# Kernel tuning notes

Measured on AMD Instinct MI355X. Metric: run time of the kernel, lower is better.

## Reference

```python
import jax, jax.numpy as jnp
import numpy as np

B, S, E = 4, 2048, 1024


def setup_inputs() -> dict:
    key = jax.random.key(0)
    ks = jax.random.split(key, 7)
    sc = 1.0 / np.sqrt(E)
    return {
        "embedded": jax.random.normal(ks[0], (B, S, E), dtype=jnp.float32),
        "Wk": jax.random.normal(ks[1], (E, E), dtype=jnp.float32) * sc,
        "bk": jax.random.normal(ks[2], (E,), dtype=jnp.float32) * 0.01,
        "Wq": jax.random.normal(ks[3], (E, E), dtype=jnp.float32) * sc,
        "bq": jax.random.normal(ks[4], (E,), dtype=jnp.float32) * 0.01,
        "Wv": jax.random.normal(ks[5], (E, E), dtype=jnp.float32) * sc,
        "bv": jax.random.normal(ks[6], (E,), dtype=jnp.float32) * 0.01,
    }


def reference(embedded, Wk, bk, Wq, bq, Wv, bv):
    # embedded: [B, S, E]
    K = embedded @ Wk.T + bk  # [B,S,E]
    Q = embedded @ Wq.T + bq
    V = embedded @ Wv.T + bv
    seq_len = K.shape[1]
    # score[b,i,j] = K_i . Q_j, scaled by 1/sqrt(seq_len) (as in original)
    scores = jnp.einsum('bie,bje->bij', K, Q) / jnp.sqrt(jnp.asarray(seq_len, K.dtype))
    # softmax over dim=-2 -> over the key index i
    W = jax.nn.softmax(scores, axis=-2)  # [B,S,S]
    # Y = (V^T @ W)^T -> Y[b,j,d] = sum_i V[b,i,d] * W[b,i,j]
    Y = jnp.einsum('bid,bij->bjd', V, W)  # [B,S,E]
    return Y
```

## Files before the change

### kernel.cpp

```cpp
#include <hip/hip_runtime.h>
#include <hip/hip_bf16.h>


typedef __bf16 bf16x8 __attribute__((ext_vector_type(8)));
typedef float  f32x4  __attribute__((ext_vector_type(4)));

__device__ __forceinline__ unsigned short f2bf(float f) {
    unsigned int u = __float_as_uint(f);
    u = (u + 0x7FFFu + ((u >> 16) & 1u)) >> 16;
    return (unsigned short)u;
}

__global__ __launch_bounds__(256)
void cvt_all(const float* __restrict__ X,  const float* __restrict__ Wq,
             const float* __restrict__ Wk, const float* __restrict__ Wv,
             unsigned short* __restrict__ Xb,  unsigned short* __restrict__ Wqb,
             unsigned short* __restrict__ Wkb, unsigned short* __restrict__ Wvb,
             float* __restrict__ l) {
    long i = (long)blockIdx.x * 256 + threadIdx.x;
    if (i < 8192) l[i] = 0.0f;
    const float* src; unsigned short* dst; long off;
    if (i < 2097152L) { src = X; dst = Xb; off = i; }
    else {
        long j = i - 2097152L;
        int w = (int)(j >> 18);
        off = j & 262143L;
        src = (w == 0) ? Wq : (w == 1) ? Wk : Wv;
        dst = (w == 0) ? Wqb : (w == 1) ? Wkb : Wvb;
    }
    float4 v = reinterpret_cast<const float4*>(src)[off];
    ushort4 o;
    o.x = f2bf(v.x); o.y = f2bf(v.y); o.z = f2bf(v.z); o.w = f2bf(v.w);
    reinterpret_cast<ushort4*>(dst)[off] = o;
}

#define GEMM_DECLS                                                      \
    const int t    = threadIdx.x;                                       \
    const int wave = t >> 6;                                            \
    const int lane = t & 63;                                            \
    const int quad = lane >> 4;                                         \
    const int lr   = lane & 15;                                         \
    const int wm   = (wave >> 1) * 64;                                  \
    const int wn   = (wave & 1) * 64;                                   \
    const int sx   = lr & 7;                                            \
    const int lrow = lane >> 3;                                         \
    const int gch  = ((lane & 7) ^ (lrow & 7)) * 8;

#define GEMM_KLOOP(Aptr, Bptr, LDA, LDB)                                \
    for (int k0 = 0; k0 < K; k0 += 64) {                                \
        _Pragma("unroll")                                               \
        for (int r = 0; r < 4; ++r) {                                   \
            const int rowb = wave * 8 + r * 32;                         \
            const int row  = rowb + lrow;                               \
            const long goffA = (long)(m0 + row) * (LDA) + k0 + gch;     \
            const long goffB = (long)(n0 + row) * (LDB) + k0 + gch;     \
            __builtin_amdgcn_global_load_lds(                           \
                (const __attribute__((address_space(1))) void*)((Aptr) + goffA), \
                (__attribute__((address_space(3))) void*)(&lsA[rowb * 64]), 16, 0, 0); \
            __builtin_amdgcn_global_load_lds(                           \
                (const __attribute__((address_space(1))) void*)((Bptr) + goffB), \
                (__attribute__((address_space(3))) void*)(&lsB[rowb * 64]), 16, 0, 0); \
        }                                                               \
        __syncthreads();                                                \
        _Pragma("unroll")                                               \
        for (int h = 0; h < 2; ++h) {                                   \
            const int cp = ((h * 4 + quad) ^ sx) * 8;                   \
            bf16x8 af[4], bfr[4];                                       \
            _Pragma("unroll")                                           \
            for (int i = 0; i < 4; ++i) {                               \
                af[i]  = __builtin_bit_cast(bf16x8,                     \
                          *reinterpret_cast<const uint4*>(&lsA[(wm + i * 16 + lr) * 64 + cp])); \
                bfr[i] = __builtin_bit_cast(bf16x8,                     \
                          *reinterpret_cast<const uint4*>(&lsB[(wn + i * 16 + lr) * 64 + cp])); \
            }                                                           \
            _Pragma("unroll")                                           \
            for (int i = 0; i < 4; ++i)                                 \
                _Pragma("unroll")                                       \
                for (int j = 0; j < 4; ++j)                             \
                    acc[i][j] = __builtin_amdgcn_mfma_f32_16x16x32_bf16(af[i], bfr[j], acc[i][j], 0, 0, 0); \
        }                                                               \
        __syncthreads();                                                \
    }

__global__ __launch_bounds__(256, 2)
void gemm_qkv(const unsigned short* __restrict__ Xb,
              const unsigned short* __restrict__ Wqb,
              const unsigned short* __restrict__ Wkb,
              const unsigned short* __restrict__ Wvb,
              const float* __restrict__ bq, const float* __restrict__ bk,
              const float* __restrict__ bv_,
              unsigned short* __restrict__ Qb, unsigned short* __restrict__ Kb,
              unsigned short* __restrict__ Vt)
{
    __shared__ unsigned short lsA[128 * 64];
    __shared__ unsigned short lsB[128 * 64];

    const int id  = blockIdx.x;
    const int g   = id & 7;
    const int jj  = id >> 3;
    const int xx  = jj & 7;
    const int yin = (jj >> 3) & 7;
    const int z   = jj >> 6;

    const unsigned short* A = Xb;
    const unsigned short* B = (z == 0) ? Wqb : (z == 1) ? Wkb : Wvb;
    const float* bias       = (z == 0) ? bq  : (z == 1) ? bk  : bv_;

    const int n0 = xx * 128;
    const int m0 = (g * 8 + yin) * 128;
    const int K = 1024;

    GEMM_DECLS
    f32x4 acc[4][4] = {};
    GEMM_KLOOP(A, B, 1024, 1024)

#pragma unroll
    for (int j = 0; j < 4; ++j) {
        const int n = n0 + wn + j * 16 + lr;
        const float bvv = bias[n];
#pragma unroll
        for (int i = 0; i < 4; ++i) {
            const int mbase = m0 + wm + i * 16 + quad * 4;
            if (z < 2) {
                unsigned short* C = (z == 0) ? Qb : Kb;
#pragma unroll
                for (int r = 0; r < 4; ++r)
                    C[(long)(mbase + r) * 1024 + n] = f2bf(acc[i][j][r] + bvv);
            } else {
                ushort4 o;
                o.x = f2bf(acc[i][j][0] + bvv);
                o.y = f2bf(acc[i][j][1] + bvv);
                o.z = f2bf(acc[i][j][2] + bvv);
                o.w = f2bf(acc[i][j][3] + bvv);
                long boff = (long)(mbase >> 11) * (1024L * 2048) + (long)n * 2048 + (mbase & 2047);
                *reinterpret_cast<ushort4*>(Vt + boff) = o;
            }
        }
    }
}

__global__ __launch_bounds__(256, 2)
void gemm_scores(const unsigned short* __restrict__ Q,
                 const unsigned short* __restrict__ Kp,
                 unsigned short* __restrict__ P, float* __restrict__ l,
                 float scale)
{
    __shared__ unsigned short lsA[128 * 64];
    __shared__ unsigned short lsB[128 * 64];

    const int id  = blockIdx.x;
    const int g   = id & 7;
    const int u   = id >> 3;
    const int bz  = g >> 1;
    const int mh  = g & 1;
    const int xx  = u & 15;
    const int yin = u >> 4;

    const unsigned short* A = Q  + (long)bz * 2048 * 1024;
    const unsigned short* B = Kp + (long)bz * 2048 * 1024;
    unsigned short* Pb = P + (long)bz * 2048 * 2048;
    float* lb = l + bz * 2048;

    const int n0 = xx * 128;
    const int m0 = (mh * 8 + yin) * 128;
    const int K = 1024;

    GEMM_DECLS
    f32x4 acc[4][4] = {};
    GEMM_KLOOP(A, B, 1024, 1024)

#pragma unroll
    for (int i = 0; i < 4; ++i) {
#pragma unroll
        for (int r = 0; r < 4; ++r) {
            const int m = m0 + wm + i * 16 + quad * 4 + r;
            float psum = 0.0f;
#pragma unroll
            for (int j = 0; j < 4; ++j) {
                const float p = __expf(acc[i][j][r] * scale);
                psum += p;
                const int n = n0 + wn + j * 16 + lr;
                Pb[(long)m * 2048 + n] = f2bf(p);
            }
#pragma unroll
            for (int o = 1; o < 16; o <<= 1) psum += __shfl_xor(psum, o, 64);
            if (lr == 0) atomicAdd(&lb[m], psum);
        }
    }
}

__global__ __launch_bounds__(256, 2)
void gemm_y(const unsigned short* __restrict__ P,
            const unsigned short* __restrict__ Vt,
            const float* __restrict__ l, float* __restrict__ out)
{
    __shared__ unsigned short lsA[128 * 64];
    __shared__ unsigned short lsB[128 * 64];

    const int id  = blockIdx.x;
    const int g   = id & 7;
    const int u   = id >> 3;
    const int bz  = g >> 1;
    const int mh  = g & 1;
    const int xx  = u & 7;
    const int yin = u >> 3;

    const unsigned short* A = P  + (long)bz * 2048 * 2048;
    const unsigned short* B = Vt + (long)bz * 1024 * 2048;
    const float* lb = l + bz * 2048;
    float* C = out + (long)bz * 2048 * 1024;

    const int n0 = xx * 128;
    const int m0 = (mh * 8 + yin) * 128;
    const int K = 2048;

    GEMM_DECLS
    f32x4 acc[4][4] = {};
    GEMM_KLOOP(A, B, 2048, 2048)

    float linv[4][4];
#pragma unroll
    for (int i = 0; i < 4; ++i)
#pragma unroll
        for (int r = 0; r < 4; ++r)
            linv[i][r] = 1.0f / lb[m0 + wm + i * 16 + quad * 4 + r];

#pragma unroll
    for (int j = 0; j < 4; ++j) {
        const int n = n0 + wn + j * 16 + lr;
#pragma unroll
        for (int i = 0; i < 4; ++i) {
            const int mbase = m0 + wm + i * 16 + quad * 4;
#pragma unroll
            for (int r = 0; r < 4; ++r)
                C[(long)(mbase + r) * 1024 + n] = acc[i][j][r] * linv[i][r];
        }
    }
}

extern "C" void kernel_launch(void* const* d_in, const int* in_sizes, int n_in,
                              void* d_out, int out_size, void* d_ws, size_t ws_size,
                              hipStream_t stream) {
    const float* X  = (const float*)d_in[0];
    const float* Wk = (const float*)d_in[1];
    const float* bk = (const float*)d_in[2];
    const float* Wq = (const float*)d_in[3];
    const float* bq = (const float*)d_in[4];
    const float* Wv = (const float*)d_in[5];
    const float* bv = (const float*)d_in[6];
    float* out = (float*)d_out;

    const size_t MB = 1024 * 1024;
    if (ws_size < 80 * MB) return;

    char* ws = (char*)d_ws;
    unsigned short* Vt  = (unsigned short*)(ws);
    unsigned short* P   = (unsigned short*)(ws + 16 * MB);
    unsigned short* Xbf = (unsigned short*)(ws + 16 * MB);
    float*          l   = (float*)(ws + 48 * MB);
    unsigned short* Wqb = (unsigned short*)(ws + 49 * MB);
    unsigned short* Wkb = (unsigned short*)(ws + 51 * MB);
    unsigned short* Wvb = (unsigned short*)(ws + 53 * MB);
    unsigned short* Qb = (unsigned short*)d_out;
    unsigned short* Kb = Qb + 8192L * 1024;

    dim3 blk(256);

    cvt_all<<<2883584 / 256, blk, 0, stream>>>(X, Wq, Wk, Wv, Xbf, Wqb, Wkb, Wvb, l);

    gemm_qkv<<<1536, blk, 0, stream>>>(Xbf, Wqb, Wkb, Wvb, bq, bk, bv, Qb, Kb, Vt);

    gemm_scores<<<1024, blk, 0, stream>>>(Qb, Kb, P, l, 0.022097086912079608f);

    gemm_y<<<512, blk, 0, stream>>>(P, Vt, l, out);
}
```

Before: 238.2 us.

## Rewrite GEMMs as 512-thread, 256-tile, double-buffered software-pipelined kernels

Replaces the simple load-sync-compute loop in all three GEMMs with a double-buffered, phase-interleaved pipeline. Each phase issues global-to-LDS loads for a later k-slice while MFMAs run, using explicit vmcnt waits, barriers and setprio. Tiles grow to 256x256 (256x128 for the output GEMM) with 8 waves per block, which raises data reuse and cuts the grid size. The cost is much larger LDS use (128 KB or 96 KB per block) and more accumulator registers, both of which may lower occupancy, plus fragile hand-written wait counts.

New measurement: 247.6 us. 1.04x slower.

```diff
diff --git a/kernel.cpp b/kernel.cpp
--- a/kernel.cpp
+++ b/kernel.cpp
@@ -34,55 +34,93 @@
     reinterpret_cast<ushort4*>(dst)[off] = o;
 }
 
-#define GEMM_DECLS                                                      \
-    const int t    = threadIdx.x;                                       \
-    const int wave = t >> 6;                                            \
-    const int lane = t & 63;                                            \
-    const int quad = lane >> 4;                                         \
-    const int lr   = lane & 15;                                         \
-    const int wm   = (wave >> 1) * 64;                                  \
-    const int wn   = (wave & 1) * 64;                                   \
-    const int sx   = lr & 7;                                            \
-    const int lrow = lane >> 3;                                         \
-    const int gch  = ((lane & 7) ^ (lrow & 7)) * 8;
-
-#define GEMM_KLOOP(Aptr, Bptr, LDA, LDB)                                \
-    for (int k0 = 0; k0 < K; k0 += 64) {                                \
-        _Pragma("unroll")                                               \
-        for (int r = 0; r < 4; ++r) {                                   \
-            const int rowb = wave * 8 + r * 32;                         \
-            const int row  = rowb + lrow;                               \
-            const long goffA = (long)(m0 + row) * (LDA) + k0 + gch;     \
-            const long goffB = (long)(n0 + row) * (LDB) + k0 + gch;     \
-            __builtin_amdgcn_global_load_lds(                           \
-                (const __attribute__((address_space(1))) void*)((Aptr) + goffA), \
-                (__attribute__((address_space(3))) void*)(&lsA[rowb * 64]), 16, 0, 0); \
-            __builtin_amdgcn_global_load_lds(                           \
-                (const __attribute__((address_space(1))) void*)((Bptr) + goffB), \
-                (__attribute__((address_space(3))) void*)(&lsB[rowb * 64]), 16, 0, 0); \
-        }                                                               \
-        __syncthreads();                                                \
-        _Pragma("unroll")                                               \
-        for (int h = 0; h < 2; ++h) {                                   \
-            const int cp = ((h * 4 + quad) ^ sx) * 8;                   \
-            bf16x8 af[4], bfr[4];                                       \
-            _Pragma("unroll")                                           \
-            for (int i = 0; i < 4; ++i) {                               \
-                af[i]  = __builtin_bit_cast(bf16x8,                     \
-                          *reinterpret_cast<const uint4*>(&lsA[(wm + i * 16 + lr) * 64 + cp])); \
-                bfr[i] = __builtin_bit_cast(bf16x8,                     \
-                          *reinterpret_cast<const uint4*>(&lsB[(wn + i * 16 + lr) * 64 + cp])); \
-            }                                                           \
-            _Pragma("unroll")                                           \
-            for (int i = 0; i < 4; ++i)                                 \
-                _Pragma("unroll")                                       \
-                for (int j = 0; j < 4; ++j)                             \
-                    acc[i][j] = __builtin_amdgcn_mfma_f32_16x16x32_bf16(af[i], bfr[j], acc[i][j], 0, 0, 0); \
-        }                                                               \
-        __syncthreads();                                                \
-    }
-
-__global__ __launch_bounds__(256, 2)
+
+#define VMW(N) asm volatile("s_waitcnt vmcnt(" #N ")" ::: "memory")
+
+#define PIPE_DECLS                                                          \
+    const int tid  = threadIdx.x;                                           \
+    const int wave = tid >> 6;                                              \
+    const int lane = tid & 63;                                              \
+    const int quad = lane >> 4;                                             \
+    const int lr   = lane & 15;                                             \
+    const int wvm  = wave >> 2;                           \
+    const int wvn  = wave & 3;                            \
+    const int rd_off = (lr >> 1) * 64 + (lr & 1) * 32                       \
+                     + ((quad ^ ((lr >> 1) & 3)) << 3);                     \
+    const int stg_rl = wave * 16 + ((lane >> 3) << 1) + ((lane >> 2) & 1);  \
+    const int stg_c  = (((lane & 3) ^ ((lane >> 3) & 3)) << 3);
+
+#define ST1(base, LD, kcol, dst, c)                                         \
+    __builtin_amdgcn_global_load_lds(                                       \
+        (const __attribute__((address_space(1))) void*)                     \
+            ((base) + (long)(c) * 128 * (LD) + (kcol)),                     \
+        (__attribute__((address_space(3))) void*)(&lds[(dst) + (c) * 4096 + wave * 512]), \
+        16, 0, 0)
+
+#define PHASE(bs, h, mh, IH_, STG, WAITS)                                   \
+    {                                                                       \
+        if ((mh) == 0) {                                                    \
+            _Pragma("unroll")                                               \
+            for (int j = 0; j < 4; ++j)                                     \
+                bfr[j] = __builtin_bit_cast(bf16x8,                         \
+                    *reinterpret_cast<const uint4*>(                        \
+                        &lds[BOFF(bs, h) + (wvn * 4 + j) * 512 + rd_off])); \
+        }                                                                   \
+        bf16x8 af[IH_];                                                     \
+        _Pragma("unroll")                                                   \
+        for (int i = 0; i < (IH_); ++i)                                     \
+            af[i] = __builtin_bit_cast(bf16x8,                              \
+                *reinterpret_cast<const uint4*>(                            \
+                    &lds[AOFF(bs, h) + (wvm * 2 * (IH_) + (mh) * (IH_) + i) * 512 + rd_off])); \
+        STG;                                                                \
+        WAITS;                                                              \
+        __builtin_amdgcn_s_barrier();                                       \
+        __builtin_amdgcn_s_setprio(1);                                      \
+        _Pragma("unroll")                                                   \
+        for (int i = 0; i < (IH_); ++i)                                     \
+            _Pragma("unroll")                                               \
+            for (int j = 0; j < 4; ++j)                                     \
+                acc[(mh) * (IH_) + i][j] = __builtin_amdgcn_mfma_f32_16x16x32_bf16( \
+                    af[i], bfr[j], acc[(mh) * (IH_) + i][j], 0, 0, 0);      \
+        __builtin_amdgcn_s_setprio(0);                                      \
+        __builtin_amdgcn_s_barrier();                                       \
+    }
+
+#define RUN_PIPELINE(IH_, NT_, WAITST)                                      \
+    f32x4 acc[2 * (IH_)][4] = {};                                           \
+    bf16x8 bfr[4];                                                          \
+    SA(0, 0, 0); SB(0, 0, 0); SA(0, 1, 0); SB(0, 1, 0); SA(1, 0, 1); SB(1, 0, 1); \
+    WAITST;                                                                 \
+    __builtin_amdgcn_s_barrier();                                           \
+    _Pragma("unroll 1")                                                     \
+    for (int it = 0; it < (NT_) / 2 - 1; ++it) {                            \
+        const int tb = 2 * it;                                              \
+        PHASE(0, 0, 0, IH_, SA(tb + 1, 1, 1), )                             \
+        PHASE(0, 0, 1, IH_, SB(tb + 1, 1, 1), )                             \
+        PHASE(0, 1, 0, IH_, SA(tb + 2, 0, 0), )                             \
+        PHASE(0, 1, 1, IH_, SB(tb + 2, 0, 0), WAITST)                       \
+        PHASE(1, 0, 0, IH_, SA(tb + 2, 1, 0), )                             \
+        PHASE(1, 0, 1, IH_, SB(tb + 2, 1, 0), )                             \
+        PHASE(1, 1, 0, IH_, SA(tb + 3, 0, 1), )                             \
+        PHASE(1, 1, 1, IH_, SB(tb + 3, 0, 1), WAITST)                       \
+    }                                                                       \
+    PHASE(0, 0, 0, IH_, SA((NT_) - 1, 1, 1), )                              \
+    PHASE(0, 0, 1, IH_, SB((NT_) - 1, 1, 1), )                              \
+    PHASE(0, 1, 0, IH_, , )                                                 \
+    PHASE(0, 1, 1, IH_, , WAITST)                                           \
+    PHASE(1, 0, 0, IH_, , )                                                 \
+    PHASE(1, 0, 1, IH_, , VMW(0))                                           \
+    PHASE(1, 1, 0, IH_, , )                                                 \
+    PHASE(1, 1, 1, IH_, , )
+
+#define AOFF(b, h) ((b) * 32768 + (h) * 8192)
+#define BOFF(b, h) ((b) * 32768 + 16384 + (h) * 8192)
+#define SA(tt, h, b) { ST1(aBase, 1024, (tt) * 64 + (h) * 32, AOFF(b, h), 0); \
+                       ST1(aBase, 1024, (tt) * 64 + (h) * 32, AOFF(b, h), 1); }
+#define SB(tt, h, b) { ST1(bBase, 1024, (tt) * 64 + (h) * 32, BOFF(b, h), 0); \
+                       ST1(bBase, 1024, (tt) * 64 + (h) * 32, BOFF(b, h), 1); }
+
+__global__ __launch_bounds__(512, 2)
 void gemm_qkv(const unsigned short* __restrict__ Xb,
               const unsigned short* __restrict__ Wqb,
               const unsigned short* __restrict__ Wkb,
@@ -92,35 +130,33 @@
               unsigned short* __restrict__ Qb, unsigned short* __restrict__ Kb,
               unsigned short* __restrict__ Vt)
 {
-    __shared__ unsigned short lsA[128 * 64];
-    __shared__ unsigned short lsB[128 * 64];
-
-    const int id  = blockIdx.x;
-    const int g   = id & 7;
-    const int jj  = id >> 3;
-    const int xx  = jj & 7;
-    const int yin = (jj >> 3) & 7;
-    const int z   = jj >> 6;
-
-    const unsigned short* A = Xb;
-    const unsigned short* B = (z == 0) ? Wqb : (z == 1) ? Wkb : Wvb;
-    const float* bias       = (z == 0) ? bq  : (z == 1) ? bk  : bv_;
-
-    const int n0 = xx * 128;
-    const int m0 = (g * 8 + yin) * 128;
-    const int K = 1024;
-
-    GEMM_DECLS
-    f32x4 acc[4][4] = {};
-    GEMM_KLOOP(A, B, 1024, 1024)
+    __shared__ __align__(16) unsigned short lds[65536];
+
+    const int id = blockIdx.x;
+    const int g  = id & 7;
+    const int u  = id >> 3;
+    const int z  = u >> 4;
+    const int w  = u & 15;
+    const int m0 = (g * 4 + (w >> 2)) * 256;
+    const int n0 = (w & 3) * 256;
+
+    const unsigned short* Aptr = Xb;
+    const unsigned short* Bptr = (z == 0) ? Wqb : (z == 1) ? Wkb : Wvb;
+    const float* bias          = (z == 0) ? bq  : (z == 1) ? bk  : bv_;
+
+    PIPE_DECLS
+    const unsigned short* aBase = Aptr + (long)(m0 + stg_rl) * 1024 + stg_c;
+    const unsigned short* bBase = Bptr + (long)(n0 + stg_rl) * 1024 + stg_c;
+
+    RUN_PIPELINE(4, 16, VMW(4))
 
 #pragma unroll
     for (int j = 0; j < 4; ++j) {
-        const int n = n0 + wn + j * 16 + lr;
+        const int n = n0 + wvn * 64 + j * 16 + lr;
         const float bvv = bias[n];
 #pragma unroll
-        for (int i = 0; i < 4; ++i) {
-            const int mbase = m0 + wm + i * 16 + quad * 4;
+        for (int i = 0; i < 8; ++i) {
+            const int mbase = m0 + wvm * 128 + i * 16 + quad * 4;
             if (z < 2) {
                 unsigned short* C = (z == 0) ? Qb : Kb;
 #pragma unroll
@@ -139,48 +175,43 @@
     }
 }
 
-__global__ __launch_bounds__(256, 2)
+__global__ __launch_bounds__(512, 2)
 void gemm_scores(const unsigned short* __restrict__ Q,
                  const unsigned short* __restrict__ Kp,
                  unsigned short* __restrict__ P, float* __restrict__ l,
                  float scale)
 {
-    __shared__ unsigned short lsA[128 * 64];
-    __shared__ unsigned short lsB[128 * 64];
-
-    const int id  = blockIdx.x;
-    const int g   = id & 7;
-    const int u   = id >> 3;
-    const int bz  = g >> 1;
-    const int mh  = g & 1;
-    const int xx  = u & 15;
-    const int yin = u >> 4;
-
-    const unsigned short* A = Q  + (long)bz * 2048 * 1024;
-    const unsigned short* B = Kp + (long)bz * 2048 * 1024;
+    __shared__ __align__(16) unsigned short lds[65536];
+
+    const int id = blockIdx.x;
+    const int g  = id & 7;
+    const int u  = id >> 3;
+    const int bz = g >> 1;
+    const int m0 = ((g & 1) * 4 + (u & 3)) * 256;
+    const int n0 = (u >> 2) * 256;
+
+    const unsigned short* Aptr = Q  + (long)bz * 2048 * 1024;
+    const unsigned short* Bptr = Kp + (long)bz * 2048 * 1024;
     unsigned short* Pb = P + (long)bz * 2048 * 2048;
     float* lb = l + bz * 2048;
 
-    const int n0 = xx * 128;
-    const int m0 = (mh * 8 + yin) * 128;
-    const int K = 1024;
-
-    GEMM_DECLS
-    f32x4 acc[4][4] = {};
-    GEMM_KLOOP(A, B, 1024, 1024)
-
-#pragma unroll
-    for (int i = 0; i < 4; ++i) {
+    PIPE_DECLS
+    const unsigned short* aBase = Aptr + (long)(m0 + stg_rl) * 1024 + stg_c;
+    const unsigned short* bBase = Bptr + (long)(n0 + stg_rl) * 1024 + stg_c;
+
+    RUN_PIPELINE(4, 16, VMW(4))
+
+#pragma unroll
+    for (int i = 0; i < 8; ++i) {
 #pragma unroll
         for (int r = 0; r < 4; ++r) {
-            const int m = m0 + wm + i * 16 + quad * 4 + r;
+            const int m = m0 + wvm * 128 + i * 16 + quad * 4 + r;
             float psum = 0.0f;
 #pragma unroll
             for (int j = 0; j < 4; ++j) {
                 const float p = __expf(acc[i][j][r] * scale);
                 psum += p;
-                const int n = n0 + wn + j * 16 + lr;
-                Pb[(long)m * 2048 + n] = f2bf(p);
+                Pb[(long)m * 2048 + (n0 + wvn * 64 + j * 16 + lr)] = f2bf(p);
             }
 #pragma unroll
             for (int o = 1; o < 16; o <<= 1) psum += __shfl_xor(psum, o, 64);
@@ -189,54 +220,66 @@
     }
 }
 
-__global__ __launch_bounds__(256, 2)
+#undef SA
+#undef SB
+#undef AOFF
+#undef BOFF
+
+#define AOFF(b, h) ((b) * 24576 + (h) * 4096)
+#define BOFF(b, h) ((b) * 24576 + 8192 + (h) * 8192)
+#define SA(tt, h, b) { ST1(aBase, 2048, (tt) * 64 + (h) * 32, AOFF(b, h), 0); }
+#define SB(tt, h, b) { ST1(bBase, 2048, (tt) * 64 + (h) * 32, BOFF(b, h), 0); \
+                       ST1(bBase, 2048, (tt) * 64 + (h) * 32, BOFF(b, h), 1); }
+
+__global__ __launch_bounds__(512, 2)
 void gemm_y(const unsigned short* __restrict__ P,
             const unsigned short* __restrict__ Vt,
             const float* __restrict__ l, float* __restrict__ out)
 {
-    __shared__ unsigned short lsA[128 * 64];
-    __shared__ unsigned short lsB[128 * 64];
-
-    const int id  = blockIdx.x;
-    const int g   = id & 7;
-    const int u   = id >> 3;
-    const int bz  = g >> 1;
-    const int mh  = g & 1;
-    const int xx  = u & 7;
-    const int yin = u >> 3;
-
-    const unsigned short* A = P  + (long)bz * 2048 * 2048;
-    const unsigned short* B = Vt + (long)bz * 1024 * 2048;
+    __shared__ __align__(16) unsigned short lds[49152];
+
+    const int id = blockIdx.x;
+    const int g  = id & 7;
+    const int u  = id >> 3;
+    const int bz = g >> 1;
+    const int m0 = ((g & 1) * 8 + (u & 7)) * 128;
+    const int n0 = (u >> 3) * 256;
+
+    const unsigned short* Aptr = P  + (long)bz * 2048 * 2048;
+    const unsigned short* Bptr = Vt + (long)bz * 1024 * 2048;
     const float* lb = l + bz * 2048;
     float* C = out + (long)bz * 2048 * 1024;
 
-    const int n0 = xx * 128;
-    const int m0 = (mh * 8 + yin) * 128;
-    const int K = 2048;
-
-    GEMM_DECLS
-    f32x4 acc[4][4] = {};
-    GEMM_KLOOP(A, B, 2048, 2048)
+    PIPE_DECLS
+    const unsigned short* aBase = Aptr + (long)(m0 + stg_rl) * 2048 + stg_c;
+    const unsigned short* bBase = Bptr + (long)(n0 + stg_rl) * 2048 + stg_c;
+
+    RUN_PIPELINE(2, 32, VMW(3))
 
     float linv[4][4];
 #pragma unroll
     for (int i = 0; i < 4; ++i)
 #pragma unroll
         for (int r = 0; r < 4; ++r)
-            linv[i][r] = 1.0f / lb[m0 + wm + i * 16 + quad * 4 + r];
+            linv[i][r] = 1.0f / lb[m0 + wvm * 64 + i * 16 + quad * 4 + r];
 
 #pragma unroll
     for (int j = 0; j < 4; ++j) {
-        const int n = n0 + wn + j * 16 + lr;
+        const int n = n0 + wvn * 64 + j * 16 + lr;
 #pragma unroll
         for (int i = 0; i < 4; ++i) {
-            const int mbase = m0 + wm + i * 16 + quad * 4;
+            const int mbase = m0 + wvm * 64 + i * 16 + quad * 4;
 #pragma unroll
             for (int r = 0; r < 4; ++r)
                 C[(long)(mbase + r) * 1024 + n] = acc[i][j][r] * linv[i][r];
         }
     }
 }
+
+#undef SA
+#undef SB
+#undef AOFF
+#undef BOFF
 
 extern "C" void kernel_launch(void* const* d_in, const int* in_sizes, int n_in,
                               void* d_out, int out_size, void* d_ws, size_t ws_size,
@@ -264,13 +307,11 @@
     unsigned short* Qb = (unsigned short*)d_out;
     unsigned short* Kb = Qb + 8192L * 1024;
 
-    dim3 blk(256);
-
-    cvt_all<<<2883584 / 256, blk, 0, stream>>>(X, Wq, Wk, Wv, Xbf, Wqb, Wkb, Wvb, l);
-
-    gemm_qkv<<<1536, blk, 0, stream>>>(Xbf, Wqb, Wkb, Wvb, bq, bk, bv, Qb, Kb, Vt);
-
-    gemm_scores<<<1024, blk, 0, stream>>>(Qb, Kb, P, l, 0.022097086912079608f);
-
-    gemm_y<<<512, blk, 0, stream>>>(P, Vt, l, out);
-}
+    cvt_all<<<2883584 / 256, dim3(256), 0, stream>>>(X, Wq, Wk, Wv, Xbf, Wqb, Wkb, Wvb, l);
+
+    gemm_qkv<<<384, dim3(512), 0, stream>>>(Xbf, Wqb, Wkb, Wvb, bq, bk, bv, Qb, Kb, Vt);
+
+    gemm_scores<<<256, dim3(512), 0, stream>>>(Qb, Kb, P, l, 0.022097086912079608f);
+
+    gemm_y<<<256, dim3(512), 0, stream>>>(P, Vt, l, out);
+}
```
